# Performance work log

Measured on AMD Instinct MI355X. Metric: run time of the kernel, lower is better.

Reference implementation:

```python
import jax, jax.numpy as jnp
import numpy as np

N_EMBED = 1024
EMBED_DIM = 64
DECAY = 0.99
EPS = 1e-05


def setup_inputs() -> dict:
    key = jax.random.key(0)
    k1, k2 = jax.random.split(key)
    z_e = jax.random.normal(k1, (16, 4096, EMBED_DIM), dtype=jnp.float32)
    # torch init: uniform_(-1/n_embed, 1/n_embed)
    embed = (jax.random.uniform(k2, (N_EMBED, EMBED_DIM), dtype=jnp.float32) * 2.0 - 1.0) / N_EMBED
    cluster_size = jnp.zeros((N_EMBED,), dtype=jnp.float32)
    embed_avg = embed.copy()
    return {"z_e": z_e, "embed": embed, "cluster_size": cluster_size, "embed_avg": embed_avg}


def reference(z_e, embed, cluster_size, embed_avg):
    B, N, E = z_e.shape
    flat = z_e.reshape(-1, E)  # [T, E], T = B*N
    dist = (jnp.sum(flat * flat, axis=1, keepdims=True)
            - 2.0 * flat @ embed.T
            + jnp.sum(embed * embed, axis=1)[None, :])  # [T, K]
    embed_ind = jnp.argmin(dist, axis=1)  # argmax(-dist)
    z_q = embed[embed_ind].reshape(B, N, E)

    # training-mode EMA statistics (scatter-add == one-hot matmul, but memory-efficient)
    onehot_sum = jnp.zeros((N_EMBED,), flat.dtype).at[embed_ind].add(1.0)
    embed_sum = jnp.zeros((N_EMBED, E), flat.dtype).at[embed_ind].add(flat)
    new_cluster_size = DECAY * cluster_size + (1.0 - DECAY) * onehot_sum
    new_embed_avg = DECAY * embed_avg + (1.0 - DECAY) * embed_sum
    n = jnp.sum(new_cluster_size)
    cs = (new_cluster_size + EPS) / (n + N_EMBED * EPS) * n
    new_embed = new_embed_avg / cs[:, None]

    diff = jnp.mean((jax.lax.stop_gradient(z_q) - z_e) ** 2)
    z_q_st = z_e + jax.lax.stop_gradient(z_q - z_e)  # straight-through
    return (z_q_st, diff, embed_ind.reshape(B, N), new_embed, new_cluster_size, new_embed_avg)
```

## Files before the change

kernel.cpp:

```cpp
#include <hip/hip_runtime.h>
#include <math.h>

#define T_TOK 65536
#define K_CODE 1024
#define E_DIM 64
#define DECAYF 0.99f
#define EPSF 1e-5f

#define TT 128
#define DWAVES 4
#define CHUNK 256
#define NCH 4
#define QCAP 2048
#define MARGIN 2.5e-3f

typedef short short8 __attribute__((ext_vector_type(8)));
typedef float f32x16 __attribute__((ext_vector_type(16)));

__device__ __forceinline__ float mul_nf(float a, float b) {
#pragma clang fp contract(off)
    return a * b;
}
__device__ __forceinline__ float add_nf(float a, float b) {
#pragma clang fp contract(off)
    return a + b;
}
__device__ __forceinline__ float sub_nf(float a, float b) {
#pragma clang fp contract(off)
    return a - b;
}

__device__ __forceinline__ float np_sq_sum64(const float* v) {
    float r[8];
#pragma unroll
    for (int j = 0; j < 8; ++j) r[j] = mul_nf(v[j], v[j]);
#pragma unroll
    for (int i = 8; i < 64; i += 8) {
#pragma unroll
        for (int j = 0; j < 8; ++j) r[j] = add_nf(r[j], mul_nf(v[i + j], v[i + j]));
    }
    float s01 = add_nf(r[0], r[1]);
    float s23 = add_nf(r[2], r[3]);
    float s45 = add_nf(r[4], r[5]);
    float s67 = add_nf(r[6], r[7]);
    return add_nf(add_nf(s01, s23), add_nf(s45, s67));
}

__device__ __forceinline__ float np_sq_row(const float* xrow) {
    const float4* xp = reinterpret_cast<const float4*>(xrow);
    float r[8];
#pragma unroll
    for (int g = 0; g < 8; ++g) {
        float4 va = xp[2 * g], vb = xp[2 * g + 1];
        float e[8] = {va.x, va.y, va.z, va.w, vb.x, vb.y, vb.z, vb.w};
#pragma unroll
        for (int j = 0; j < 8; ++j) {
            if (g == 0) r[j] = mul_nf(e[j], e[j]);
            else        r[j] = add_nf(r[j], mul_nf(e[j], e[j]));
        }
    }
    float s01 = add_nf(r[0], r[1]);
    float s23 = add_nf(r[2], r[3]);
    float s45 = add_nf(r[4], r[5]);
    float s67 = add_nf(r[6], r[7]);
    return add_nf(add_nf(s01, s23), add_nf(s45, s67));
}

__device__ __forceinline__ unsigned short f2bf_rne(float f) {
    unsigned u = __float_as_uint(f);
    u += 0x7FFFu + ((u >> 16) & 1u);
    return (unsigned short)(u >> 16);
}


__global__ __launch_bounds__(256) void wnorm_kernel(const float* __restrict__ embed,
                                                    float* __restrict__ wnorm,
                                                    unsigned short* __restrict__ w16) {
    int k = blockIdx.x * 256 + threadIdx.x;
    if (k < K_CODE) {
        float w[64];
        const float4* wp = reinterpret_cast<const float4*>(embed + (size_t)k * E_DIM);
#pragma unroll
        for (int i = 0; i < 16; ++i) {
            float4 v = wp[i];
            w[4 * i + 0] = v.x; w[4 * i + 1] = v.y; w[4 * i + 2] = v.z; w[4 * i + 3] = v.w;
        }
        wnorm[k] = np_sq_sum64(w);
        unsigned short* wr = w16 + (size_t)k * E_DIM;
#pragma unroll
        for (int i = 0; i < 64; ++i) wr[i] = f2bf_rne(w[i]);
    }
}

__device__ __forceinline__ void exact_key(int t0, int tl, int code,
                                          const float* __restrict__ z_e,
                                          const float* __restrict__ embed,
                                          const float* xn_s, const float* wn_s,
                                          unsigned long long* key_s) {
    const float4* xp = reinterpret_cast<const float4*>(z_e + (size_t)(t0 + tl) * E_DIM);
    const float4* wp = reinterpret_cast<const float4*>(embed + (size_t)code * E_DIM);
    float d = 0.f;
#pragma unroll
    for (int m = 0; m < 16; ++m) {
        float4 x4 = xp[m];
        float4 w4 = wp[m];
        d = __builtin_fmaf(x4.x, w4.x, d);
        d = __builtin_fmaf(x4.y, w4.y, d);
        d = __builtin_fmaf(x4.z, w4.z, d);
        d = __builtin_fmaf(x4.w, w4.w, d);
    }
    float dist = add_nf(sub_nf(xn_s[tl], d + d), wn_s[code]);
    unsigned b = __float_as_uint(dist);
    unsigned mk = (b & 0x80000000u) ? ~b : (b | 0x80000000u);
    atomicMin(key_s + tl, ((unsigned long long)mk << 32) | (unsigned)code);
}

__global__ __launch_bounds__(256) void dist_kernel(const float* __restrict__ z_e,
                                                   const float* __restrict__ embed,
                                                   const float* __restrict__ wnorm,
                                                   const unsigned short* __restrict__ w16,
                                                   unsigned long long* __restrict__ keys_g) {
    __shared__ unsigned short Wb[2][CHUNK * E_DIM];
    __shared__ float wn_s[K_CODE];
    __shared__ float xn_s[TT];
    __shared__ unsigned long long key_s[TT];
    __shared__ unsigned q_s[QCAP];
    __shared__ int qc_s;

    int tid = threadIdx.x;
    int lane = tid & 63;
    int wave = tid >> 6;
    int g = lane >> 5;
    int t0 = blockIdx.x * TT;

    if (tid < TT) key_s[tid] = ~0ull;
    if (tid == 0) qc_s = 0;
    *reinterpret_cast<float4*>(&wn_s[tid * 4]) =
        *reinterpret_cast<const float4*>(&wnorm[tid * 4]);
    if (tid < TT) xn_s[tid] = np_sq_row(z_e + (size_t)(t0 + tid) * E_DIM);

    int arow = wave * 32 + (lane & 31);
    const float* xrow = z_e + (size_t)(t0 + arow) * E_DIM;
    short8 afr[4];
#pragma unroll
    for (int kc = 0; kc < 4; ++kc) {
        int base = kc * 16 + g * 8;
        float4 a = *reinterpret_cast<const float4*>(xrow + base);
        float4 b = *reinterpret_cast<const float4*>(xrow + base + 4);
        afr[kc][0] = (short)f2bf_rne(a.x);
        afr[kc][1] = (short)f2bf_rne(a.y);
        afr[kc][2] = (short)f2bf_rne(a.z);
        afr[kc][3] = (short)f2bf_rne(a.w);
        afr[kc][4] = (short)f2bf_rne(b.x);
        afr[kc][5] = (short)f2bf_rne(b.y);
        afr[kc][6] = (short)f2bf_rne(b.z);
        afr[kc][7] = (short)f2bf_rne(b.w);
    }

    const uint4* w16q = reinterpret_cast<const uint4*>(w16);

    {
        uint4 st[8];
#pragma unroll
        for (int it = 0; it < 8; ++it) {
            int idx = it * 256 + tid;
            int cl = idx >> 3, ps = idx & 7;
            int ls = ps ^ (cl & 7);
            st[it] = w16q[(size_t)cl * 8 + ls];
        }
#pragma unroll
        for (int it = 0; it < 8; ++it)
            reinterpret_cast<uint4*>(Wb[0])[it * 256 + tid] = st[it];
    }
    __syncthreads();

    float xnr[16];
#pragma unroll
    for (int r = 0; r < 16; ++r) {
        int row = (r & 3) + 8 * (r >> 2) + 4 * g;
        xnr[r] = xn_s[wave * 32 + row];
    }
    float minr[16];
#pragma unroll
    for (int r = 0; r < 16; ++r) minr[r] = INFINITY;

    for (int ph = 0; ph < 2 * NCH; ++ph) {
        int cur = ph & 1;
        int cbase = (ph & 3) * CHUNK;
        uint4 st[8];
        if (ph < 2 * NCH - 1) {
            int ncb = ((ph + 1) & 3) * CHUNK;
#pragma unroll
            for (int it = 0; it < 8; ++it) {
                int idx = it * 256 + tid;
                int cl = idx >> 3, ps = idx & 7;
                int ls = ps ^ (cl & 7);
                st[it] = w16q[(size_t)(ncb + cl) * 8 + ls];
            }
        }
        int pass = ph >> 2;
        for (int tile = 0; tile < 8; ++tile) {
            int cloc = tile * 32 + (lane & 31);
            float wn_c = wn_s[cbase + cloc];
            f32x16 acc;
#pragma unroll
            for (int i = 0; i < 16; ++i) acc[i] = 0.f;
#pragma unroll
            for (int kc = 0; kc < 4; ++kc) {
                int ps = (2 * kc + g) ^ (cloc & 7);
                short8 bfr = *reinterpret_cast<const short8*>(
                    &Wb[cur][cloc * E_DIM + ps * 8]);
                acc = __builtin_amdgcn_mfma_f32_32x32x16_bf16(afr[kc], bfr, acc, 0, 0, 0);
            }
            if (pass == 0) {
#pragma unroll
                for (int r = 0; r < 16; ++r) {
                    float dist = __builtin_fmaf(acc[r], -2.0f, xnr[r] + wn_c);
                    minr[r] = fminf(minr[r], dist);
                }
            } else {
                float tmin = INFINITY;
#pragma unroll
                for (int r = 0; r < 16; ++r) {
                    float dist = __builtin_fmaf(acc[r], -2.0f, xnr[r] + wn_c);
                    tmin = fminf(tmin, dist - minr[r]);
                }
                if (tmin <= MARGIN) {
#pragma unroll
                    for (int r = 0; r < 16; ++r) {
                        float dist = __builtin_fmaf(acc[r], -2.0f, xnr[r] + wn_c);
                        if (dist <= minr[r] + MARGIN) {
                            int row = (r & 3) + 8 * (r >> 2) + 4 * g;
                            int tl = wave * 32 + row;
                            int code = cbase + cloc;
                            int slot = atomicAdd(&qc_s, 1);
                            if (slot < QCAP)
                                q_s[slot] = ((unsigned)tl << 10) | (unsigned)code;
                            else
                                exact_key(t0, tl, code, z_e, embed, xn_s, wn_s, key_s);
                        }
                    }
                }
            }
        }
        if (ph == NCH - 1) {
#pragma unroll
            for (int off = 1; off < 32; off <<= 1) {
#pragma unroll
                for (int r = 0; r < 16; ++r)
                    minr[r] = fminf(minr[r], __shfl_xor(minr[r], off, 64));
            }
        }
        if (ph < 2 * NCH - 1) {
#pragma unroll
            for (int it = 0; it < 8; ++it)
                reinterpret_cast<uint4*>(Wb[cur ^ 1])[it * 256 + tid] = st[it];
        }
        __syncthreads();
    }

    int qn = qc_s;
    if (qn > QCAP) qn = QCAP;
    for (int e = tid; e < qn; e += 256) {
        unsigned q = q_s[e];
        int tl = (int)(q >> 10);
        int code = (int)(q & 1023u);
        exact_key(t0, tl, code, z_e, embed, xn_s, wn_s, key_s);
    }
    __syncthreads();
    if (tid < TT) keys_g[t0 + tid] = key_s[tid];
}

__global__ __launch_bounds__(256) void combine_kernel(const float* __restrict__ z_e,
                                                      const float* __restrict__ embed,
                                                      const unsigned long long* __restrict__ keys,
                                                      float* __restrict__ out_zq,
                                                      float* __restrict__ out_ind,
                                                      float* __restrict__ diff_acc,
                                                      float* __restrict__ esum_rep,
                                                      float* __restrict__ onehot_rep,
                                                      int rep_mask) {
    __shared__ int sidx[64];
    __shared__ float sred[4];
    int tid = threadIdx.x;
    int t0 = blockIdx.x * 64;

    if (tid < 64) {
        unsigned long long kv = keys[t0 + tid];
        int bi = (int)(kv & 0x3FFull);
        sidx[tid] = bi;
        out_ind[t0 + tid] = (float)bi;
    }
    __syncthreads();

    float ds = 0.f;
#pragma unroll
    for (int u = 0; u < 4; ++u) {
        int v = u * 256 + tid;
        int tl = v >> 4;
        int c = v & 15;
        int bi = sidx[tl];
        float4 w4 = *reinterpret_cast<const float4*>(embed + (size_t)bi * E_DIM + c * 4);
        float4 x4 = *reinterpret_cast<const float4*>(z_e + (size_t)(t0 + tl) * E_DIM + c * 4);
        float rx = sub_nf(w4.x, x4.x);
        float ry = sub_nf(w4.y, x4.y);
        float rz = sub_nf(w4.z, x4.z);
        float rw = sub_nf(w4.w, x4.w);
        float4 o;
        o.x = add_nf(x4.x, rx);
        o.y = add_nf(x4.y, ry);
        o.z = add_nf(x4.z, rz);
        o.w = add_nf(x4.w, rw);
        *reinterpret_cast<float4*>(out_zq + (size_t)(t0 + tl) * E_DIM + c * 4) = o;
        ds = __builtin_fmaf(rx, rx, ds);
        ds = __builtin_fmaf(ry, ry, ds);
        ds = __builtin_fmaf(rz, rz, ds);
        ds = __builtin_fmaf(rw, rw, ds);
    }
#pragma unroll
    for (int o = 32; o > 0; o >>= 1) ds += __shfl_down(ds, o, 64);
    if ((tid & 63) == 0) sred[tid >> 6] = ds;
    __syncthreads();
    if (tid == 0) atomicAdd(diff_acc, sred[0] + sred[1] + sred[2] + sred[3]);

    int lane = tid & 63;
    int wv = tid >> 6;
    int rep = blockIdx.x & rep_mask;
    float* esum = esum_rep + (size_t)rep * (K_CODE * E_DIM);
    float* onehot = onehot_rep + (size_t)rep * K_CODE;
#pragma unroll
    for (int j = 0; j < 16; ++j) {
        int tl = wv * 16 + j;
        int bi = sidx[tl];
        float xv = z_e[(size_t)(t0 + tl) * E_DIM + lane];
        atomicAdd(&esum[(size_t)bi * E_DIM + lane], xv);
        if (lane == 0) atomicAdd(&onehot[bi], 1.0f);
    }
}

__global__ __launch_bounds__(1024) void finalize_cs_kernel(const float* __restrict__ cluster_size,
                                                           const float* __restrict__ onehot_rep,
                                                           const float* __restrict__ ws_diff,
                                                           float* __restrict__ out_diff,
                                                           float* __restrict__ out_ncs,
                                                           float* __restrict__ ws_n,
                                                           int nrep) {
    int k = threadIdx.x;
    float oh = 0.f;
    for (int r = 0; r < nrep; ++r) oh += onehot_rep[(size_t)r * K_CODE + k];
    float ncs = DECAYF * cluster_size[k] + (1.0f - DECAYF) * oh;
    out_ncs[k] = ncs;

    __shared__ float red[1024];
    red[k] = ncs;
    __syncthreads();
#pragma unroll
    for (int s = 512; s > 0; s >>= 1) {
        if (k < s) red[k] += red[k + s];
        __syncthreads();
    }
    if (k == 0) {
        ws_n[0] = red[0];
        out_diff[0] = ws_diff[0] * (1.0f / 4194304.0f);
    }
}

__global__ __launch_bounds__(256) void finalize_embed_kernel(const float* __restrict__ embed_avg,
                                                             const float* __restrict__ esum_rep,
                                                             const float* __restrict__ out_ncs,
                                                             const float* __restrict__ ws_n,
                                                             float* __restrict__ out_ne,
                                                             float* __restrict__ out_nea,
                                                             int nrep) {
    int gid = blockIdx.x * 256 + threadIdx.x;
    int k = gid >> 4;
    int c = gid & 15;
    float n = ws_n[0];
    float ncs = out_ncs[k];
    float cs = (ncs + EPSF) / (n + (float)K_CODE * EPSF) * n;

    size_t off = (size_t)k * E_DIM + (size_t)c * 4;
    float4 s4 = make_float4(0.f, 0.f, 0.f, 0.f);
    for (int r = 0; r < nrep; ++r) {
        float4 v = *reinterpret_cast<const float4*>(esum_rep + (size_t)r * (K_CODE * E_DIM) + off);
        s4.x += v.x; s4.y += v.y; s4.z += v.z; s4.w += v.w;
    }
    float4 a = *reinterpret_cast<const float4*>(embed_avg + off);
    float4 nea, ne;
    nea.x = DECAYF * a.x + (1.0f - DECAYF) * s4.x;
    nea.y = DECAYF * a.y + (1.0f - DECAYF) * s4.y;
    nea.z = DECAYF * a.z + (1.0f - DECAYF) * s4.z;
    nea.w = DECAYF * a.w + (1.0f - DECAYF) * s4.w;
    ne.x = nea.x / cs; ne.y = nea.y / cs; ne.z = nea.z / cs; ne.w = nea.w / cs;
    *reinterpret_cast<float4*>(out_nea + off) = nea;
    *reinterpret_cast<float4*>(out_ne + off) = ne;
}

extern "C" void kernel_launch(void* const* d_in, const int* in_sizes, int n_in,
                              void* d_out, int out_size, void* d_ws, size_t ws_size,
                              hipStream_t stream) {
    const float* z_e = (const float*)d_in[0];
    const float* embed = (const float*)d_in[1];
    const float* cluster_size = (const float*)d_in[2];
    const float* embed_avg = (const float*)d_in[3];

    float* out = (float*)d_out;
    float* o_zq = out;
    float* o_diff = out + 4194304;
    float* o_ind = out + 4194305;
    float* o_ne = out + 4194305 + 65536;
    float* o_ncs = o_ne + 65536;
    float* o_nea = o_ncs + 1024;

    float* ws = (float*)d_ws;
    float* ws_wnorm = ws;
    float* ws_diff = ws + 1024;
    float* ws_n = ws + 1025;
    unsigned long long* ws_keys = (unsigned long long*)(ws + 2048);
    float* ws_onehot = ws + 133120;
    unsigned short* ws_w16 = (unsigned short*)(ws + 141312);
    float* ws_esum = ws + 174080;

    int nrep = 1;
    while (nrep < 8 &&
           ws_size >= (size_t)(174080 + (size_t)(2 * nrep) * 65536) * sizeof(float))
        nrep *= 2;

    hipMemsetAsync(ws + 1024, 0, 2 * sizeof(float), stream);
    hipMemsetAsync(ws_onehot, 0, (size_t)(8192 + (size_t)nrep * 65536) * sizeof(float),
                   stream);

    wnorm_kernel<<<4, 256, 0, stream>>>(embed, ws_wnorm, ws_w16);
    dist_kernel<<<T_TOK / TT, 256, 0, stream>>>(z_e, embed, ws_wnorm, ws_w16, ws_keys);
    combine_kernel<<<1024, 256, 0, stream>>>(z_e, embed, ws_keys, o_zq, o_ind, ws_diff,
                                             ws_esum, ws_onehot, nrep - 1);
    finalize_cs_kernel<<<1, 1024, 0, stream>>>(cluster_size, ws_onehot, ws_diff,
                                               o_diff, o_ncs, ws_n, nrep);
    finalize_embed_kernel<<<64, 256, 0, stream>>>(embed_avg, ws_esum, o_ncs, ws_n,
                                                  o_ne, o_nea, nrep);
}
```

Before: 199.9 us.

## Fuse combine into distance kernel and keep full bf16 codebook in LDS

```diff
diff --git a/kernel.cpp b/kernel.cpp
--- a/kernel.cpp
+++ b/kernel.cpp
@@ -7,10 +7,7 @@
 #define DECAYF 0.99f
 #define EPSF 1e-5f
 
-#define TT 128
-#define DWAVES 4
-#define CHUNK 256
-#define NCH 4
+#define TT 256
 #define QCAP 2048
 #define MARGIN 2.5e-3f
 
@@ -66,10 +63,10 @@
     return add_nf(add_nf(s01, s23), add_nf(s45, s67));
 }
 
-__device__ __forceinline__ unsigned short f2bf_rne(float f) {
+__device__ __forceinline__ unsigned f2bf_rne(float f) {
     unsigned u = __float_as_uint(f);
     u += 0x7FFFu + ((u >> 16) & 1u);
-    return (unsigned short)(u >> 16);
+    return (u >> 16);
 }
 
 
@@ -86,9 +83,14 @@
             w[4 * i + 0] = v.x; w[4 * i + 1] = v.y; w[4 * i + 2] = v.z; w[4 * i + 3] = v.w;
         }
         wnorm[k] = np_sq_sum64(w);
-        unsigned short* wr = w16 + (size_t)k * E_DIM;
-#pragma unroll
-        for (int i = 0; i < 64; ++i) wr[i] = f2bf_rne(w[i]);
+        unsigned uu[32];
+#pragma unroll
+        for (int i = 0; i < 32; ++i)
+            uu[i] = f2bf_rne(w[2 * i]) | (f2bf_rne(w[2 * i + 1]) << 16);
+        uint4* wq = reinterpret_cast<uint4*>(w16 + (size_t)k * E_DIM);
+#pragma unroll
+        for (int q = 0; q < 8; ++q)
+            wq[q] = make_uint4(uu[4 * q], uu[4 * q + 1], uu[4 * q + 2], uu[4 * q + 3]);
     }
 }
 
@@ -115,12 +117,17 @@
     atomicMin(key_s + tl, ((unsigned long long)mk << 32) | (unsigned)code);
 }
 
-__global__ __launch_bounds__(256) void dist_kernel(const float* __restrict__ z_e,
+__global__ __launch_bounds__(512) void dist_kernel(const float* __restrict__ z_e,
                                                    const float* __restrict__ embed,
                                                    const float* __restrict__ wnorm,
                                                    const unsigned short* __restrict__ w16,
-                                                   unsigned long long* __restrict__ keys_g) {
-    __shared__ unsigned short Wb[2][CHUNK * E_DIM];
+                                                   float* __restrict__ out_zq,
+                                                   float* __restrict__ out_ind,
+                                                   float* __restrict__ diff_acc,
+                                                   float* __restrict__ esum_rep,
+                                                   float* __restrict__ onehot_rep,
+                                                   int rep_mask) {
+    __shared__ unsigned short Ws[K_CODE * E_DIM];
     __shared__ float wn_s[K_CODE];
     __shared__ float xn_s[TT];
     __shared__ unsigned long long key_s[TT];
@@ -135,9 +142,20 @@
 
     if (tid < TT) key_s[tid] = ~0ull;
     if (tid == 0) qc_s = 0;
-    *reinterpret_cast<float4*>(&wn_s[tid * 4]) =
-        *reinterpret_cast<const float4*>(&wnorm[tid * 4]);
+    *reinterpret_cast<float2*>(&wn_s[tid * 2]) =
+        *reinterpret_cast<const float2*>(&wnorm[tid * 2]);
     if (tid < TT) xn_s[tid] = np_sq_row(z_e + (size_t)(t0 + tid) * E_DIM);
+
+    {
+        const uint4* wq = reinterpret_cast<const uint4*>(w16);
+        uint4* WsQ = reinterpret_cast<uint4*>(Ws);
+#pragma unroll
+        for (int it = 0; it < 16; ++it) {
+            int idx = it * 512 + tid;
+            int cl = idx >> 3, ps = idx & 7;
+            WsQ[cl * 8 + ps] = wq[(size_t)cl * 8 + (ps ^ (cl & 7))];
+        }
+    }
 
     int arow = wave * 32 + (lane & 31);
     const float* xrow = z_e + (size_t)(t0 + arow) * E_DIM;
@@ -157,21 +175,6 @@
         afr[kc][7] = (short)f2bf_rne(b.w);
     }
 
-    const uint4* w16q = reinterpret_cast<const uint4*>(w16);
-
-    {
-        uint4 st[8];
-#pragma unroll
-        for (int it = 0; it < 8; ++it) {
-            int idx = it * 256 + tid;
-            int cl = idx >> 3, ps = idx & 7;
-            int ls = ps ^ (cl & 7);
-            st[it] = w16q[(size_t)cl * 8 + ls];
-        }
-#pragma unroll
-        for (int it = 0; it < 8; ++it)
-            reinterpret_cast<uint4*>(Wb[0])[it * 256 + tid] = st[it];
-    }
     __syncthreads();
 
     float xnr[16];
@@ -184,158 +187,102 @@
 #pragma unroll
     for (int r = 0; r < 16; ++r) minr[r] = INFINITY;
 
-    for (int ph = 0; ph < 2 * NCH; ++ph) {
-        int cur = ph & 1;
-        int cbase = (ph & 3) * CHUNK;
-        uint4 st[8];
-        if (ph < 2 * NCH - 1) {
-            int ncb = ((ph + 1) & 3) * CHUNK;
-#pragma unroll
-            for (int it = 0; it < 8; ++it) {
-                int idx = it * 256 + tid;
-                int cl = idx >> 3, ps = idx & 7;
-                int ls = ps ^ (cl & 7);
-                st[it] = w16q[(size_t)(ncb + cl) * 8 + ls];
-            }
-        }
-        int pass = ph >> 2;
-        for (int tile = 0; tile < 8; ++tile) {
-            int cloc = tile * 32 + (lane & 31);
-            float wn_c = wn_s[cbase + cloc];
-            f32x16 acc;
-#pragma unroll
-            for (int i = 0; i < 16; ++i) acc[i] = 0.f;
-#pragma unroll
-            for (int kc = 0; kc < 4; ++kc) {
-                int ps = (2 * kc + g) ^ (cloc & 7);
-                short8 bfr = *reinterpret_cast<const short8*>(
-                    &Wb[cur][cloc * E_DIM + ps * 8]);
-                acc = __builtin_amdgcn_mfma_f32_32x32x16_bf16(afr[kc], bfr, acc, 0, 0, 0);
-            }
-            if (pass == 0) {
-#pragma unroll
-                for (int r = 0; r < 16; ++r) {
-                    float dist = __builtin_fmaf(acc[r], -2.0f, xnr[r] + wn_c);
-                    minr[r] = fminf(minr[r], dist);
-                }
-            } else {
-                float tmin = INFINITY;
-#pragma unroll
-                for (int r = 0; r < 16; ++r) {
-                    float dist = __builtin_fmaf(acc[r], -2.0f, xnr[r] + wn_c);
-                    tmin = fminf(tmin, dist - minr[r]);
-                }
-                if (tmin <= MARGIN) {
-#pragma unroll
-                    for (int r = 0; r < 16; ++r) {
-                        float dist = __builtin_fmaf(acc[r], -2.0f, xnr[r] + wn_c);
-                        if (dist <= minr[r] + MARGIN) {
-                            int row = (r & 3) + 8 * (r >> 2) + 4 * g;
-                            int tl = wave * 32 + row;
-                            int code = cbase + cloc;
-                            int slot = atomicAdd(&qc_s, 1);
-                            if (slot < QCAP)
-                                q_s[slot] = ((unsigned)tl << 10) | (unsigned)code;
-                            else
-                                exact_key(t0, tl, code, z_e, embed, xn_s, wn_s, key_s);
-                        }
-                    }
+#pragma unroll 2
+    for (int tile = 0; tile < 32; ++tile) {
+        int code = tile * 32 + (lane & 31);
+        float wn_c = wn_s[code];
+        f32x16 acc;
+#pragma unroll
+        for (int i = 0; i < 16; ++i) acc[i] = 0.f;
+#pragma unroll
+        for (int kc = 0; kc < 4; ++kc) {
+            int ps = (2 * kc + g) ^ (code & 7);
+            short8 bfr = *reinterpret_cast<const short8*>(&Ws[code * E_DIM + ps * 8]);
+            acc = __builtin_amdgcn_mfma_f32_32x32x16_bf16(afr[kc], bfr, acc, 0, 0, 0);
+        }
+#pragma unroll
+        for (int r = 0; r < 16; ++r) {
+            float dist = __builtin_fmaf(acc[r], -2.0f, xnr[r] + wn_c);
+            minr[r] = fminf(minr[r], dist);
+        }
+    }
+
+#pragma unroll
+    for (int off = 1; off < 32; off <<= 1) {
+#pragma unroll
+        for (int r = 0; r < 16; ++r)
+            minr[r] = fminf(minr[r], __shfl_xor(minr[r], off, 64));
+    }
+
+#pragma unroll 2
+    for (int tile = 0; tile < 32; ++tile) {
+        int code = tile * 32 + (lane & 31);
+        float wn_c = wn_s[code];
+        f32x16 acc;
+#pragma unroll
+        for (int i = 0; i < 16; ++i) acc[i] = 0.f;
+#pragma unroll
+        for (int kc = 0; kc < 4; ++kc) {
+            int ps = (2 * kc + g) ^ (code & 7);
+            short8 bfr = *reinterpret_cast<const short8*>(&Ws[code * E_DIM + ps * 8]);
+            acc = __builtin_amdgcn_mfma_f32_32x32x16_bf16(afr[kc], bfr, acc, 0, 0, 0);
+        }
+        float tmin = INFINITY;
+#pragma unroll
+        for (int r = 0; r < 16; ++r) {
+            float dist = __builtin_fmaf(acc[r], -2.0f, xnr[r] + wn_c);
+            tmin = fminf(tmin, dist - minr[r]);
+        }
+        if (tmin <= MARGIN) {
+#pragma unroll
+            for (int r = 0; r < 16; ++r) {
+                float dist = __builtin_fmaf(acc[r], -2.0f, xnr[r] + wn_c);
+                if (dist <= minr[r] + MARGIN) {
+                    int row = (r & 3) + 8 * (r >> 2) + 4 * g;
+                    int tl = wave * 32 + row;
+                    int slot = atomicAdd(&qc_s, 1);
+                    if (slot < QCAP)
+                        q_s[slot] = ((unsigned)tl << 10) | (unsigned)code;
+                    else
+                        exact_key(t0, tl, code, z_e, embed, xn_s, wn_s, key_s);
                 }
             }
         }
-        if (ph == NCH - 1) {
-#pragma unroll
-            for (int off = 1; off < 32; off <<= 1) {
-#pragma unroll
-                for (int r = 0; r < 16; ++r)
-                    minr[r] = fminf(minr[r], __shfl_xor(minr[r], off, 64));
-            }
-        }
-        if (ph < 2 * NCH - 1) {
-#pragma unroll
-            for (int it = 0; it < 8; ++it)
-                reinterpret_cast<uint4*>(Wb[cur ^ 1])[it * 256 + tid] = st[it];
-        }
-        __syncthreads();
-    }
+    }
+    __syncthreads();
 
     int qn = qc_s;
     if (qn > QCAP) qn = QCAP;
-    for (int e = tid; e < qn; e += 256) {
+    for (int e = tid; e < qn; e += 512) {
         unsigned q = q_s[e];
         int tl = (int)(q >> 10);
         int code = (int)(q & 1023u);
         exact_key(t0, tl, code, z_e, embed, xn_s, wn_s, key_s);
     }
     __syncthreads();
-    if (tid < TT) keys_g[t0 + tid] = key_s[tid];
-}
-
-__global__ __launch_bounds__(256) void combine_kernel(const float* __restrict__ z_e,
-                                                      const float* __restrict__ embed,
-                                                      const unsigned long long* __restrict__ keys,
-                                                      float* __restrict__ out_zq,
-                                                      float* __restrict__ out_ind,
-                                                      float* __restrict__ diff_acc,
-                                                      float* __restrict__ esum_rep,
-                                                      float* __restrict__ onehot_rep,
-                                                      int rep_mask) {
-    __shared__ int sidx[64];
-    __shared__ float sred[4];
-    int tid = threadIdx.x;
-    int t0 = blockIdx.x * 64;
-
-    if (tid < 64) {
-        unsigned long long kv = keys[t0 + tid];
-        int bi = (int)(kv & 0x3FFull);
-        sidx[tid] = bi;
-        out_ind[t0 + tid] = (float)bi;
-    }
-    __syncthreads();
-
-    float ds = 0.f;
-#pragma unroll
-    for (int u = 0; u < 4; ++u) {
-        int v = u * 256 + tid;
-        int tl = v >> 4;
-        int c = v & 15;
-        int bi = sidx[tl];
-        float4 w4 = *reinterpret_cast<const float4*>(embed + (size_t)bi * E_DIM + c * 4);
-        float4 x4 = *reinterpret_cast<const float4*>(z_e + (size_t)(t0 + tl) * E_DIM + c * 4);
-        float rx = sub_nf(w4.x, x4.x);
-        float ry = sub_nf(w4.y, x4.y);
-        float rz = sub_nf(w4.z, x4.z);
-        float rw = sub_nf(w4.w, x4.w);
-        float4 o;
-        o.x = add_nf(x4.x, rx);
-        o.y = add_nf(x4.y, ry);
-        o.z = add_nf(x4.z, rz);
-        o.w = add_nf(x4.w, rw);
-        *reinterpret_cast<float4*>(out_zq + (size_t)(t0 + tl) * E_DIM + c * 4) = o;
-        ds = __builtin_fmaf(rx, rx, ds);
-        ds = __builtin_fmaf(ry, ry, ds);
-        ds = __builtin_fmaf(rz, rz, ds);
-        ds = __builtin_fmaf(rw, rw, ds);
-    }
-#pragma unroll
-    for (int o = 32; o > 0; o >>= 1) ds += __shfl_down(ds, o, 64);
-    if ((tid & 63) == 0) sred[tid >> 6] = ds;
-    __syncthreads();
-    if (tid == 0) atomicAdd(diff_acc, sred[0] + sred[1] + sred[2] + sred[3]);
-
-    int lane = tid & 63;
-    int wv = tid >> 6;
+
+    if (tid < TT) out_ind[t0 + tid] = (float)(unsigned)(key_s[tid] & 1023ull);
+
     int rep = blockIdx.x & rep_mask;
     float* esum = esum_rep + (size_t)rep * (K_CODE * E_DIM);
     float* onehot = onehot_rep + (size_t)rep * K_CODE;
-#pragma unroll
-    for (int j = 0; j < 16; ++j) {
-        int tl = wv * 16 + j;
-        int bi = sidx[tl];
+
+    float ds = 0.f;
+#pragma unroll 4
+    for (int it = 0; it < 32; ++it) {
+        int tl = wave * 32 + it;
+        int bi = (int)(unsigned)(key_s[tl] & 1023ull);
         float xv = z_e[(size_t)(t0 + tl) * E_DIM + lane];
+        float wv = embed[(size_t)bi * E_DIM + lane];
+        float rr = sub_nf(wv, xv);
+        out_zq[(size_t)(t0 + tl) * E_DIM + lane] = add_nf(xv, rr);
+        ds = __builtin_fmaf(rr, rr, ds);
         atomicAdd(&esum[(size_t)bi * E_DIM + lane], xv);
         if (lane == 0) atomicAdd(&onehot[bi], 1.0f);
     }
+#pragma unroll
+    for (int o = 32; o > 0; o >>= 1) ds += __shfl_down(ds, o, 64);
+    if (lane == 0) atomicAdd(diff_acc, ds);
 }
 
 __global__ __launch_bounds__(1024) void finalize_cs_kernel(const float* __restrict__ cluster_size,
@@ -414,26 +361,24 @@
 
     float* ws = (float*)d_ws;
     float* ws_wnorm = ws;
-    float* ws_diff = ws + 1024;
-    float* ws_n = ws + 1025;
-    unsigned long long* ws_keys = (unsigned long long*)(ws + 2048);
-    float* ws_onehot = ws + 133120;
-    unsigned short* ws_w16 = (unsigned short*)(ws + 141312);
-    float* ws_esum = ws + 174080;
+    unsigned short* ws_w16 = (unsigned short*)(ws + 1024);
+    float* ws_diff = ws + 33792;
+    float* ws_n = ws + 33793;
+    float* ws_onehot = ws + 33796;
+    float* ws_esum = ws + 41988;
 
     int nrep = 1;
     while (nrep < 8 &&
-           ws_size >= (size_t)(174080 + (size_t)(2 * nrep) * 65536) * sizeof(float))
+           (size_t)(41988 + (size_t)(2 * nrep) * 65536) * sizeof(float) <= ws_size)
         nrep *= 2;
 
-    hipMemsetAsync(ws + 1024, 0, 2 * sizeof(float), stream);
-    hipMemsetAsync(ws_onehot, 0, (size_t)(8192 + (size_t)nrep * 65536) * sizeof(float),
-                   stream);
+    hipMemsetAsync(ws + 33792, 0,
+                   (size_t)(4 + 8192 + (size_t)nrep * 65536) * sizeof(float), stream);
 
     wnorm_kernel<<<4, 256, 0, stream>>>(embed, ws_wnorm, ws_w16);
-    dist_kernel<<<T_TOK / TT, 256, 0, stream>>>(z_e, embed, ws_wnorm, ws_w16, ws_keys);
-    combine_kernel<<<1024, 256, 0, stream>>>(z_e, embed, ws_keys, o_zq, o_ind, ws_diff,
-                                             ws_esum, ws_onehot, nrep - 1);
+    dist_kernel<<<T_TOK / TT, 512, 0, stream>>>(z_e, embed, ws_wnorm, ws_w16,
+                                                o_zq, o_ind, ws_diff,
+                                                ws_esum, ws_onehot, nrep - 1);
     finalize_cs_kernel<<<1, 1024, 0, stream>>>(cluster_size, ws_onehot, ws_diff,
                                                o_diff, o_ncs, ws_n, nrep);
     finalize_embed_kernel<<<64, 256, 0, stream>>>(embed_avg, ws_esum, o_ncs, ws_n,
```

Result: faster. 181.7 us (-9.1%).
